# Kernel optimization log

Measured on AMD Instinct MI355X. Metric: run time of the kernel, lower is better.

## Reference

```python
import jax, jax.numpy as jnp
import numpy as np

B, T, D, H = 4, 1024, 1024, 16


def setup_inputs() -> dict:
    key = jax.random.key(0)
    ks = jax.random.split(key, 8)
    s = 0.02
    return {
        "query": jax.random.normal(ks[0], (B, T, D), jnp.float32),
        "key": jax.random.normal(ks[1], (B, T, D), jnp.float32),
        "values": jax.random.normal(ks[2], (B, T, D), jnp.float32),
        "Wq": jax.random.normal(ks[3], (D, D), jnp.float32) * s,
        "bq": jnp.zeros((D,), jnp.float32),
        "Wv": jax.random.normal(ks[4], (D, D), jnp.float32) * s,
        "bv": jnp.zeros((D,), jnp.float32),
        "Wo": jax.random.normal(ks[5], (D, D), jnp.float32) * s,
        "bo": jnp.zeros((D,), jnp.float32),
        "gammas": jax.random.normal(ks[6], (H,), jnp.float32) * 0.1,
        "ln_g": jnp.ones((D,), jnp.float32),
        "ln_b": jnp.zeros((D,), jnp.float32),
    }


def _layer(query, key, values, Wq, bq, Wv, bv, Wo, bo, gammas, ln_g, ln_b):
    b, t, d = query.shape
    h = gammas.shape[0]
    dk = d // h

    def proj(x, W, bias):  # torch Linear: x @ W.T + b, then split heads -> (b,h,t,dk)
        y = jnp.einsum('btd,ed->bte', x, W) + bias
        return y.reshape(b, t, h, dk).transpose(0, 2, 1, 3)

    q = proj(query, Wq, bq)
    k = proj(key, Wq, bq)   # kq_same=True
    v = proj(values, Wv, bv)

    scores = jnp.einsum('bhqd,bhkd->bhqk', q, k) / np.float32(np.sqrt(dk))
    idx = jnp.arange(t)
    pos = jnp.abs(idx[:, None] - idx[None, :]).astype(scores.dtype)  # |i-j|, (t,t)
    mask = idx[:, None] > idx[None, :]  # strict lower tril (peek_cur=False)
    neg = jnp.asarray(-1e32, scores.dtype)

    # gamma time-effect (computed without grad in original)
    s_ = jax.nn.softmax(jnp.where(mask, scores, neg), axis=-1)
    distcum = jnp.cumsum(s_, axis=-1)
    disttotal = jnp.sum(s_, axis=-1, keepdims=True)
    dist = jnp.sqrt(jnp.clip((disttotal - distcum) * pos, 0.0, None))
    dist = jax.lax.stop_gradient(dist)
    gamma_eff = -jnp.abs(gammas)[None, :, None, None]  # (1,h,1,1)
    total_effect = jnp.clip(jnp.exp(dist * gamma_eff), 1e-5, 1e5)
    scores = scores * total_effect

    p = jax.nn.softmax(jnp.where(mask, scores, neg), axis=-1)
    p = jnp.where(mask, p, 0.0)
    # maxout rescale (maxout=True since peek_cur=False)
    scale = jnp.minimum(1.0 / jnp.max(p, axis=-1, keepdims=True), 5.0)
    p = p * scale

    out = jnp.einsum('bhqk,bhkd->bhqd', p, v)
    concat = out.transpose(0, 2, 1, 3).reshape(b, t, d)
    attn_out = jnp.einsum('btd,ed->bte', concat, Wo) + bo

    x = query + attn_out  # residual (dropout is identity in eval)
    mu = jnp.mean(x, axis=-1, keepdims=True)
    var = jnp.var(x, axis=-1, keepdims=True)
    return (x - mu) / jnp.sqrt(var + 1e-5) * ln_g + ln_b


def reference(query, key, values, Wq, bq, Wv, bv, Wo, bo, gammas, ln_g, ln_b):
    return _layer(query, key, values, Wq, bq, Wv, bv, Wo, bo, gammas, ln_g, ln_b)
```

## Files before the change

### kernel.cpp

```cpp
#include <hip/hip_runtime.h>
#include <hip/hip_bf16.h>
#include <stdint.h>


typedef unsigned short ushort_t;
typedef __attribute__((ext_vector_type(8))) short short8;
typedef __attribute__((ext_vector_type(8))) unsigned short u16x8;
typedef __attribute__((ext_vector_type(4))) float f32x4;
typedef __attribute__((ext_vector_type(4))) unsigned short u16x4;

#define GLB_CAST(p) ((const __attribute__((address_space(1))) void*)(p))
#define LDS_CAST(p) ((__attribute__((address_space(3))) void*)(p))

#if __has_builtin(__builtin_amdgcn_exp2f)
#define EXP2F(x) __builtin_amdgcn_exp2f(x)
#else
#define EXP2F(x) exp2f(x)
#endif

#define LOG2E 1.44269504f

__device__ __forceinline__ float b2f(ushort_t u) {
  union { unsigned int i; float f; } x; x.i = ((unsigned int)u) << 16; return x.f;
}
__device__ __forceinline__ ushort_t f2b(float f) {
  __hip_bfloat16 h = __float2bfloat16(f);
  return *reinterpret_cast<ushort_t*>(&h);
}
__device__ __forceinline__ float wave_sum(float v) {
  #pragma unroll
  for (int d = 32; d > 0; d >>= 1) v += __shfl_xor(v, d);
  return v;
}

__global__ void conv6_f32_bf16(const float* __restrict__ s0, const float* __restrict__ s1,
                               const float* __restrict__ s2, const float* __restrict__ s3,
                               const float* __restrict__ s4, const float* __restrict__ s5,
                               ushort_t* __restrict__ d0, ushort_t* __restrict__ d1,
                               ushort_t* __restrict__ d2, ushort_t* __restrict__ d3,
                               ushort_t* __restrict__ d4, ushort_t* __restrict__ d5,
                               int n4tok, int n4w) {
  const int y = blockIdx.y;
  const float* srcs[6] = {s0, s1, s2, s3, s4, s5};
  ushort_t*    dsts[6] = {d0, d1, d2, d3, d4, d5};
  const int n4 = (y < 3) ? n4tok : n4w;
  int i = blockIdx.x * blockDim.x + threadIdx.x;
  if (i < n4) {
    const float4 v = reinterpret_cast<const float4*>(srcs[y])[i];
    u16x4 o;
    o[0] = f2b(v.x); o[1] = f2b(v.y); o[2] = f2b(v.z); o[3] = f2b(v.w);
    reinterpret_cast<u16x4*>(dsts[y])[i] = o;
  }
}

__device__ __forceinline__ void gemm_core(const ushort_t* __restrict__ A,
                                          const ushort_t* __restrict__ Bt,
                                          int m0, int n0,
                                          ushort_t* As, ushort_t* Bs,
                                          f32x4 (&acc)[4][4]) {
  const int tid = threadIdx.x, lane = tid & 63;
  const int wid = tid >> 6;
  const int wr = (wid >> 1) * 64, wc = (wid & 1) * 64;
  for (int k0 = 0; k0 < 1024; k0 += 32) {
    #pragma unroll
    for (int it = 0; it < 2; ++it) {
      const int idx = tid * 8 + it * 2048;
      const int r = idx >> 5, kk = idx & 31;
      __builtin_amdgcn_global_load_lds(GLB_CAST(&A[(size_t)(m0 + r) * 1024 + k0 + kk]),
                                       LDS_CAST(&As[idx]), 16, 0, 0);
      __builtin_amdgcn_global_load_lds(GLB_CAST(&Bt[(size_t)(n0 + r) * 1024 + k0 + kk]),
                                       LDS_CAST(&Bs[idx]), 16, 0, 0);
    }
    __syncthreads();
    short8 af[4], bfv[4];
    #pragma unroll
    for (int m = 0; m < 4; ++m)
      af[m] = *reinterpret_cast<const short8*>(&As[(wr + m * 16 + (lane & 15)) * 32 + (lane >> 4) * 8]);
    #pragma unroll
    for (int n = 0; n < 4; ++n)
      bfv[n] = *reinterpret_cast<const short8*>(&Bs[(wc + n * 16 + (lane & 15)) * 32 + (lane >> 4) * 8]);
    #pragma unroll
    for (int m = 0; m < 4; ++m)
      #pragma unroll
      for (int n = 0; n < 4; ++n)
        acc[m][n] = __builtin_amdgcn_mfma_f32_16x16x32_bf16(af[m], bfv[n], acc[m][n], 0, 0, 0);
    __syncthreads();
  }
}

__global__ __launch_bounds__(256) void gemm_proj(
    const ushort_t* __restrict__ qb, const ushort_t* __restrict__ kb, const ushort_t* __restrict__ vb,
    const ushort_t* __restrict__ Wqb, const ushort_t* __restrict__ Wvb,
    const float* __restrict__ bq, const float* __restrict__ bvv,
    ushort_t* __restrict__ Qh, ushort_t* __restrict__ Kh, ushort_t* __restrict__ Vt) {
  __shared__ ushort_t As[128 * 32], Bs[128 * 32];
  const ushort_t* A; const ushort_t* Bt; const float* bias;
  if (blockIdx.z == 0)      { A = qb; Bt = Wqb; bias = bq;  }
  else if (blockIdx.z == 1) { A = kb; Bt = Wqb; bias = bq;  }
  else                      { A = vb; Bt = Wvb; bias = bvv; }
  const int m0 = blockIdx.y * 128, n0 = blockIdx.x * 128;
  f32x4 zero = {0.f, 0.f, 0.f, 0.f};
  f32x4 acc[4][4];
  #pragma unroll
  for (int m = 0; m < 4; ++m)
    #pragma unroll
    for (int n = 0; n < 4; ++n) acc[m][n] = zero;
  gemm_core(A, Bt, m0, n0, As, Bs, acc);
  const int lane = threadIdx.x & 63, wid = threadIdx.x >> 6;
  const int wr = (wid >> 1) * 64, wc = (wid & 1) * 64;
  if (blockIdx.z == 2) {
    #pragma unroll
    for (int m = 0; m < 4; ++m)
      #pragma unroll
      for (int n = 0; n < 4; ++n) {
        const int rowb = m0 + wr + m * 16 + (lane >> 4) * 4;
        const int col  = n0 + wc + n * 16 + (lane & 15);
        u16x4 pk;
        #pragma unroll
        for (int r4 = 0; r4 < 4; ++r4) pk[r4] = f2b(acc[m][n][r4] + bias[col]);
        const int bi = rowb >> 10, t = rowb & 1023;
        *reinterpret_cast<u16x4*>(
            &Vt[((size_t)(bi * 16 + (col >> 6)) * 64 + (col & 63)) * 1024 + t]) = pk;
      }
  } else {
    ushort_t* dst = (blockIdx.z == 0) ? Qh : Kh;
    #pragma unroll
    for (int m = 0; m < 4; ++m)
      #pragma unroll
      for (int n = 0; n < 4; ++n)
        #pragma unroll
        for (int r4 = 0; r4 < 4; ++r4) {
          const int row = m0 + wr + m * 16 + (lane >> 4) * 4 + r4;
          const int col = n0 + wc + n * 16 + (lane & 15);
          const float v = acc[m][n][r4] + bias[col];
          const int bi = row >> 10, t = row & 1023, h = col >> 6, dd = col & 63;
          dst[((size_t)(bi * 16 + h) * 1024 + t) * 64 + dd] = f2b(v);
        }
  }
}

__global__ __launch_bounds__(256) void gemm_out(
    const ushort_t* __restrict__ A, const ushort_t* __restrict__ Bt,
    const float* __restrict__ bias, const float* __restrict__ resid,
    float* __restrict__ dstF) {
  __shared__ ushort_t As[128 * 32], Bs[128 * 32];
  const int m0 = blockIdx.y * 128, n0 = blockIdx.x * 128;
  f32x4 zero = {0.f, 0.f, 0.f, 0.f};
  f32x4 acc[4][4];
  #pragma unroll
  for (int m = 0; m < 4; ++m)
    #pragma unroll
    for (int n = 0; n < 4; ++n) acc[m][n] = zero;
  gemm_core(A, Bt, m0, n0, As, Bs, acc);
  const int lane = threadIdx.x & 63, wid = threadIdx.x >> 6;
  const int wr = (wid >> 1) * 64, wc = (wid & 1) * 64;
  #pragma unroll
  for (int m = 0; m < 4; ++m)
    #pragma unroll
    for (int n = 0; n < 4; ++n)
      #pragma unroll
      for (int r4 = 0; r4 < 4; ++r4) {
        const int row = m0 + wr + m * 16 + (lane >> 4) * 4 + r4;
        const int col = n0 + wc + n * 16 + (lane & 15);
        const size_t o = (size_t)row * 1024 + col;
        dstF[o] = acc[m][n][r4] + bias[col] + resid[o];
      }
}

template<int CH>
__device__ __forceinline__ void phase_b(ushort_t* __restrict__ Sb, const int i0,
                                        const int w, const int lane, const float gamx) {
  const int c0 = CH * lane;
  int idxA = 0, idxB = 0;
  if constexpr (CH == 16) {
    const int ca = 2 * lane, cb = 2 * lane + 1;
    idxA = (ca ^ ((ca >> 3) & 7)) << 3;
    idxB = (cb ^ ((cb >> 3) & 7)) << 3;
  } else {
    const int c = c0 >> 3;
    idxA = ((c ^ ((c >> 3) & 7)) << 3) + (c0 & 7);
  }
  #pragma unroll
  for (int rr = 0; rr < 2; ++rr) {
    const int r = w * 2 + rr;
    const int i = i0 + r;
    ushort_t* __restrict__ Row = &Sb[r * 1032];
    if (i == 0) {
      #pragma unroll
      for (int e = 0; e < CH; ++e) {
        if constexpr (CH == 16) Row[(e < 8) ? (idxA + e) : (idxB + e - 8)] = 0;
        else                    Row[idxA + e] = 0;
      }
      continue;
    }
    float s[CH];
    if constexpr (CH == 16) {
      const u16x8 ra = *reinterpret_cast<const u16x8*>(&Row[idxA]);
      const u16x8 rb = *reinterpret_cast<const u16x8*>(&Row[idxB]);
      #pragma unroll
      for (int e = 0; e < 8; ++e) { s[e] = b2f(ra[e]); s[8 + e] = b2f(rb[e]); }
    } else if constexpr (CH == 8) {
      const u16x8 ra = *reinterpret_cast<const u16x8*>(&Row[idxA]);
      #pragma unroll
      for (int e = 0; e < 8; ++e) s[e] = b2f(ra[e]);
    } else if constexpr (CH == 4) {
      const u16x4 ra = *reinterpret_cast<const u16x4*>(&Row[idxA]);
      #pragma unroll
      for (int e = 0; e < 4; ++e) s[e] = b2f(ra[e]);
    } else if constexpr (CH == 2) {
      s[0] = b2f(Row[idxA]); s[1] = b2f(Row[idxA + 1]);
    } else {
      s[0] = b2f(Row[idxA]);
    }
    const int nact = min(max(i - c0, 0), CH);
    #pragma unroll
    for (int e = 0; e < CH; ++e)
      s[e] = (e < nact) ? s[e] * LOG2E : -__builtin_inff();
    float ev[CH];
    float run = 0.f;
    #pragma unroll
    for (int e = 0; e < CH; ++e) { ev[e] = EXP2F(s[e]); run += ev[e]; }
    float v = run;
    #pragma unroll
    for (int d = 1; d < 64; d <<= 1) {
      const float t = __shfl_down(v, d);
      v += (lane + d < 64) ? t : 0.f;
    }
    const float Z1 = __shfl(v, 0);
    const float excl = v - run;
    const float g2 = -gamx * rsqrtf(Z1);
    const float posb = (float)(i - c0);
    float run2 = excl;
    #pragma unroll
    for (int e = CH - 1; e >= 0; --e) {
      const float t = fmaxf(run2 * (posb - (float)e), 0.f);
      run2 += ev[e];
      const float eff = fmaxf(EXP2F(g2 * sqrtf(t)), 1e-5f);
      s[e] *= eff;
    }
    float z2 = 0.f, mm = 0.f;
    #pragma unroll
    for (int e = 0; e < CH; ++e) {
      ev[e] = EXP2F(s[e]);
      z2 += ev[e];
      mm = fmaxf(mm, ev[e]);
    }
    #pragma unroll
    for (int d = 32; d > 0; d >>= 1) {
      z2 += __shfl_xor(z2, d);
      mm = fmaxf(mm, __shfl_xor(mm, d));
    }
    const float sc = fminf(1.f / mm, 5.f / z2);
    if constexpr (CH == 16) {
      u16x8 oa, ob;
      #pragma unroll
      for (int e = 0; e < 8; ++e) { oa[e] = f2b(ev[e] * sc); ob[e] = f2b(ev[8 + e] * sc); }
      *reinterpret_cast<u16x8*>(&Row[idxA]) = oa;
      *reinterpret_cast<u16x8*>(&Row[idxB]) = ob;
    } else if constexpr (CH == 8) {
      u16x8 oa;
      #pragma unroll
      for (int e = 0; e < 8; ++e) oa[e] = f2b(ev[e] * sc);
      *reinterpret_cast<u16x8*>(&Row[idxA]) = oa;
    } else if constexpr (CH == 4) {
      u16x4 oa;
      #pragma unroll
      for (int e = 0; e < 4; ++e) oa[e] = f2b(ev[e] * sc);
      *reinterpret_cast<u16x4*>(&Row[idxA]) = oa;
    } else if constexpr (CH == 2) {
      Row[idxA] = f2b(ev[0] * sc); Row[idxA + 1] = f2b(ev[1] * sc);
    } else {
      Row[idxA] = f2b(ev[0] * sc);
    }
  }
}

__global__ __launch_bounds__(512, 6) void attn_kernel(
    const ushort_t* __restrict__ Qh, const ushort_t* __restrict__ Kh,
    const ushort_t* __restrict__ Vt, const float* __restrict__ gammas,
    ushort_t* __restrict__ concat) {
  __shared__ __align__(16) ushort_t Sb[16 * 1032];
  __shared__ __align__(16) ushort_t Qs[16 * 72];
  const int tid = threadIdx.x, lane = tid & 63, w = tid >> 6;
  const int bh = blockIdx.y, bi = bh >> 4, h = bh & 15;
  const int i0 = blockIdx.x * 16;
  const size_t base = (size_t)bh * (1024 * 64);

  if (tid < 256) {
    const int r = tid >> 4, d = (tid & 15) * 4;
    *reinterpret_cast<u16x4*>(&Qs[r * 72 + d]) =
        *reinterpret_cast<const u16x4*>(&Qh[base + (size_t)(i0 + r) * 64 + d]);
  }
  __syncthreads();

  const int upper = i0 + 16;
  for (int nt = 0; nt < 8; ++nt) {
    const int colbase = (nt * 8 + w) * 16;
    if (colbase >= upper) break;
    f32x4 acc = {0.f, 0.f, 0.f, 0.f};
    #pragma unroll
    for (int kt = 0; kt < 2; ++kt) {
      const short8 a = *reinterpret_cast<const short8*>(
          &Qs[(lane & 15) * 72 + kt * 32 + (lane >> 4) * 8]);
      const short8 bb = *reinterpret_cast<const short8*>(
          &Kh[base + (size_t)(colbase + (lane & 15)) * 64 + kt * 32 + (lane >> 4) * 8]);
      acc = __builtin_amdgcn_mfma_f32_16x16x32_bf16(a, bb, acc, 0, 0, 0);
    }
    const int j = colbase + (lane & 15);
    const int cq = (j >> 3) ^ ((j >> 6) & 7);
    const int ub = cq * 8 + (j & 7);
    #pragma unroll
    for (int r4 = 0; r4 < 4; ++r4) {
      const int rf = (lane >> 4) * 4 + r4;
      Sb[rf * 1032 + ub] = f2b(acc[r4] * 0.125f);
    }
  }
  __syncthreads();

  const float gamx = fabsf(gammas[h]) * LOG2E;
  const int chp = (upper + 63) >> 6;
  if (chp == 1)      phase_b<1>(Sb, i0, w, lane, gamx);
  else if (chp == 2) phase_b<2>(Sb, i0, w, lane, gamx);
  else if (chp <= 4) phase_b<4>(Sb, i0, w, lane, gamx);
  else if (chp <= 8) phase_b<8>(Sb, i0, w, lane, gamx);
  else               phase_b<16>(Sb, i0, w, lane, gamx);
  __syncthreads();

  if (w < 4) {
    const int d0 = w * 16;
    const int arow = lane & 15;
    const ushort_t* Prow = &Sb[arow * 1032];
    const ushort_t* Vrow = Vt + base + (size_t)(d0 + arow) * 1024;
    const int kmax = (upper + 31) & ~31;
    f32x4 acc = {0.f, 0.f, 0.f, 0.f};
    for (int k0 = 0; k0 < kmax; k0 += 32) {
      const int c = (k0 >> 3) + (lane >> 4);
      const int cq = c ^ ((c >> 3) & 7);
      const short8 a = *reinterpret_cast<const short8*>(&Prow[cq * 8]);
      const short8 bb = *reinterpret_cast<const short8*>(&Vrow[k0 + (lane >> 4) * 8]);
      acc = __builtin_amdgcn_mfma_f32_16x16x32_bf16(a, bb, acc, 0, 0, 0);
    }
    #pragma unroll
    for (int r4 = 0; r4 < 4; ++r4) {
      const int row = (lane >> 4) * 4 + r4;
      const int i = i0 + row;
      concat[((size_t)(bi * 1024 + i)) * 1024 + h * 64 + d0 + arow] = f2b(acc[r4]);
    }
  }
}

__global__ __launch_bounds__(256) void ln_kernel(const float* __restrict__ x,
                                                 const float* __restrict__ g,
                                                 const float* __restrict__ bb,
                                                 float* __restrict__ out) {
  const int row = blockIdx.x, tid = threadIdx.x, lane = tid & 63, w = tid >> 6;
  const float4 v = reinterpret_cast<const float4*>(x + (size_t)row * 1024)[tid];
  float s = v.x + v.y + v.z + v.w;
  float q = v.x * v.x + v.y * v.y + v.z * v.z + v.w * v.w;
  s = wave_sum(s); q = wave_sum(q);
  __shared__ float ps[4], pq[4];
  if (lane == 0) { ps[w] = s; pq[w] = q; }
  __syncthreads();
  const float ts = ps[0] + ps[1] + ps[2] + ps[3];
  const float tq = pq[0] + pq[1] + pq[2] + pq[3];
  const float mu = ts * (1.f / 1024.f);
  const float inv = rsqrtf(tq * (1.f / 1024.f) - mu * mu + 1e-5f);
  const float4 gv = reinterpret_cast<const float4*>(g)[tid];
  const float4 bv = reinterpret_cast<const float4*>(bb)[tid];
  float4 o;
  o.x = (v.x - mu) * inv * gv.x + bv.x;
  o.y = (v.y - mu) * inv * gv.y + bv.y;
  o.z = (v.z - mu) * inv * gv.z + bv.z;
  o.w = (v.w - mu) * inv * gv.w + bv.w;
  reinterpret_cast<float4*>(out + (size_t)row * 1024)[tid] = o;
}

extern "C" void kernel_launch(void* const* d_in, const int* in_sizes, int n_in,
                              void* d_out, int out_size, void* d_ws, size_t ws_size,
                              hipStream_t stream) {
  (void)in_sizes; (void)n_in; (void)out_size; (void)ws_size;
  const float* query  = (const float*)d_in[0];
  const float* key    = (const float*)d_in[1];
  const float* values = (const float*)d_in[2];
  const float* Wq     = (const float*)d_in[3];
  const float* bq     = (const float*)d_in[4];
  const float* Wv     = (const float*)d_in[5];
  const float* bv     = (const float*)d_in[6];
  const float* Wo     = (const float*)d_in[7];
  const float* bo     = (const float*)d_in[8];
  const float* gammas = (const float*)d_in[9];
  const float* ln_g   = (const float*)d_in[10];
  const float* ln_b   = (const float*)d_in[11];
  float* out = (float*)d_out;

  const size_t NT = 4096ull * 1024;
  const size_t NW = 1024ull * 1024;
  char* p = (char*)d_ws;
  ushort_t* qb  = (ushort_t*)p; p += NT * 2;
  ushort_t* kb  = (ushort_t*)p; p += NT * 2;
  ushort_t* vb  = (ushort_t*)p; p += NT * 2;
  ushort_t* Wqb = (ushort_t*)p; p += NW * 2;
  ushort_t* Wvb = (ushort_t*)p; p += NW * 2;
  ushort_t* Wob = (ushort_t*)p; p += NW * 2;
  ushort_t* Qh  = (ushort_t*)p; p += NT * 2;
  ushort_t* Kh  = (ushort_t*)p; p += NT * 2;
  ushort_t* Vt  = (ushort_t*)p; p += NT * 2;
  ushort_t* concat = vb;
  float*    xbuf   = (float*)qb;

  conv6_f32_bf16<<<dim3(4096, 6), 256, 0, stream>>>(
      query, key, values, Wq, Wv, Wo, qb, kb, vb, Wqb, Wvb, Wob,
      (int)(NT / 4), (int)(NW / 4));

  gemm_proj<<<dim3(8, 32, 3), 256, 0, stream>>>(qb, kb, vb, Wqb, Wvb, bq, bv, Qh, Kh, Vt);
  attn_kernel<<<dim3(64, 64), 512, 0, stream>>>(Qh, Kh, Vt, gammas, concat);
  gemm_out<<<dim3(8, 32), 256, 0, stream>>>(concat, Wob, bo, query, xbuf);
  ln_kernel<<<4096, 256, 0, stream>>>(xbuf, ln_g, ln_b, out);
}
```

Baseline: 190.7 us.

## Shrink attention blocks to 256 threads, recompute exps, and remap block order

```diff
diff --git a/kernel.cpp b/kernel.cpp
--- a/kernel.cpp
+++ b/kernel.cpp
@@ -180,9 +180,8 @@
     const int c = c0 >> 3;
     idxA = ((c ^ ((c >> 3) & 7)) << 3) + (c0 & 7);
   }
-  #pragma unroll
-  for (int rr = 0; rr < 2; ++rr) {
-    const int r = w * 2 + rr;
+  for (int rr = 0; rr < 4; ++rr) {
+    const int r = w * 4 + rr;
     const int i = i0 + r;
     ushort_t* __restrict__ Row = &Sb[r * 1032];
     if (i == 0) {
@@ -213,13 +212,12 @@
       s[0] = b2f(Row[idxA]);
     }
     const int nact = min(max(i - c0, 0), CH);
-    #pragma unroll
-    for (int e = 0; e < CH; ++e)
+    float run = 0.f;
+    #pragma unroll
+    for (int e = 0; e < CH; ++e) {
       s[e] = (e < nact) ? s[e] * LOG2E : -__builtin_inff();
-    float ev[CH];
-    float run = 0.f;
-    #pragma unroll
-    for (int e = 0; e < CH; ++e) { ev[e] = EXP2F(s[e]); run += ev[e]; }
+      run += EXP2F(s[e]);
+    }
     float v = run;
     #pragma unroll
     for (int d = 1; d < 64; d <<= 1) {
@@ -234,16 +232,16 @@
     #pragma unroll
     for (int e = CH - 1; e >= 0; --e) {
       const float t = fmaxf(run2 * (posb - (float)e), 0.f);
-      run2 += ev[e];
+      run2 += EXP2F(s[e]);
       const float eff = fmaxf(EXP2F(g2 * sqrtf(t)), 1e-5f);
       s[e] *= eff;
     }
     float z2 = 0.f, mm = 0.f;
     #pragma unroll
     for (int e = 0; e < CH; ++e) {
-      ev[e] = EXP2F(s[e]);
-      z2 += ev[e];
-      mm = fmaxf(mm, ev[e]);
+      const float p = EXP2F(s[e]);
+      z2 += p;
+      mm = fmaxf(mm, p);
     }
     #pragma unroll
     for (int d = 32; d > 0; d >>= 1) {
@@ -254,39 +252,44 @@
     if constexpr (CH == 16) {
       u16x8 oa, ob;
       #pragma unroll
-      for (int e = 0; e < 8; ++e) { oa[e] = f2b(ev[e] * sc); ob[e] = f2b(ev[8 + e] * sc); }
+      for (int e = 0; e < 8; ++e) {
+        oa[e] = f2b(EXP2F(s[e]) * sc);
+        ob[e] = f2b(EXP2F(s[8 + e]) * sc);
+      }
       *reinterpret_cast<u16x8*>(&Row[idxA]) = oa;
       *reinterpret_cast<u16x8*>(&Row[idxB]) = ob;
     } else if constexpr (CH == 8) {
       u16x8 oa;
       #pragma unroll
-      for (int e = 0; e < 8; ++e) oa[e] = f2b(ev[e] * sc);
+      for (int e = 0; e < 8; ++e) oa[e] = f2b(EXP2F(s[e]) * sc);
       *reinterpret_cast<u16x8*>(&Row[idxA]) = oa;
     } else if constexpr (CH == 4) {
       u16x4 oa;
       #pragma unroll
-      for (int e = 0; e < 4; ++e) oa[e] = f2b(ev[e] * sc);
+      for (int e = 0; e < 4; ++e) oa[e] = f2b(EXP2F(s[e]) * sc);
       *reinterpret_cast<u16x4*>(&Row[idxA]) = oa;
     } else if constexpr (CH == 2) {
-      Row[idxA] = f2b(ev[0] * sc); Row[idxA + 1] = f2b(ev[1] * sc);
+      Row[idxA] = f2b(EXP2F(s[0]) * sc); Row[idxA + 1] = f2b(EXP2F(s[1]) * sc);
     } else {
-      Row[idxA] = f2b(ev[0] * sc);
-    }
-  }
-}
-
-__global__ __launch_bounds__(512, 6) void attn_kernel(
+      Row[idxA] = f2b(EXP2F(s[0]) * sc);
+    }
+  }
+}
+
+__global__ __launch_bounds__(256, 4) void attn_kernel(
     const ushort_t* __restrict__ Qh, const ushort_t* __restrict__ Kh,
     const ushort_t* __restrict__ Vt, const float* __restrict__ gammas,
     ushort_t* __restrict__ concat) {
   __shared__ __align__(16) ushort_t Sb[16 * 1032];
   __shared__ __align__(16) ushort_t Qs[16 * 72];
   const int tid = threadIdx.x, lane = tid & 63, w = tid >> 6;
-  const int bh = blockIdx.y, bi = bh >> 4, h = bh & 15;
-  const int i0 = blockIdx.x * 16;
+  const int flat = blockIdx.x + (blockIdx.y << 6);
+  const int bh = ((flat & 7) << 3) | (flat >> 9);
+  const int i0 = ((flat >> 3) & 63) << 4;
+  const int bi = bh >> 4, h = bh & 15;
   const size_t base = (size_t)bh * (1024 * 64);
 
-  if (tid < 256) {
+  {
     const int r = tid >> 4, d = (tid & 15) * 4;
     *reinterpret_cast<u16x4*>(&Qs[r * 72 + d]) =
         *reinterpret_cast<const u16x4*>(&Qh[base + (size_t)(i0 + r) * 64 + d]);
@@ -294,8 +297,8 @@
   __syncthreads();
 
   const int upper = i0 + 16;
-  for (int nt = 0; nt < 8; ++nt) {
-    const int colbase = (nt * 8 + w) * 16;
+  for (int nt = 0; nt < 16; ++nt) {
+    const int colbase = (nt * 4 + w) * 16;
     if (colbase >= upper) break;
     f32x4 acc = {0.f, 0.f, 0.f, 0.f};
     #pragma unroll
@@ -326,7 +329,7 @@
   else               phase_b<16>(Sb, i0, w, lane, gamx);
   __syncthreads();
 
-  if (w < 4) {
+  {
     const int d0 = w * 16;
     const int arow = lane & 15;
     const ushort_t* Prow = &Sb[arow * 1032];
@@ -413,7 +416,7 @@
       (int)(NT / 4), (int)(NW / 4));
 
   gemm_proj<<<dim3(8, 32, 3), 256, 0, stream>>>(qb, kb, vb, Wqb, Wvb, bq, bv, Qh, Kh, Vt);
-  attn_kernel<<<dim3(64, 64), 512, 0, stream>>>(Qh, Kh, Vt, gammas, concat);
+  attn_kernel<<<dim3(64, 64), 256, 0, stream>>>(Qh, Kh, Vt, gammas, concat);
   gemm_out<<<dim3(8, 32), 256, 0, stream>>>(concat, Wob, bo, query, xbuf);
   ln_kernel<<<4096, 256, 0, stream>>>(xbuf, ln_g, ln_b, out);
 }
```

After: 181.0 us. 5.1% less time.
